# Kernel tuning notes

Hardware: AMD Instinct MI355X
Metric: run time of the kernel (lower is better)

The kernel has to match this reference:

```python
import jax, jax.numpy as jnp
import numpy as np

POOL = 14  # pool_size


def setup_inputs() -> dict:
    key = jax.random.key(0)
    k1, k2, k3, k4, k5 = jax.random.split(key, 5)
    H = W = 128
    C = 1024
    R = 256  # num_rois
    img = jax.random.normal(k1, (1, H, W, C), dtype=jnp.float32)
    # valid integer boxes (x1,y1,x2,y2) with x2>x1, y2>y1, inside the map
    x1 = jax.random.randint(k2, (R,), 0, W // 2)
    y1 = jax.random.randint(k3, (R,), 0, H // 2)
    bw = jax.random.randint(k4, (R,), 4, W // 2)
    bh = jax.random.randint(k5, (R,), 4, H // 2)
    rois = jnp.stack([x1, y1, x1 + bw, y1 + bh], axis=1).astype(jnp.float32)[None]  # [1,R,4]
    return {"img": img, "rois": rois}


def _roi_resize(img, rois, pool):
    # img: [1,H,W,C], rois: [1,R,4] float (x1,y1,x2,y2)
    H, W = img.shape[1], img.shape[2]
    fmap = img[0]  # [H,W,C]
    r = rois[0].astype(jnp.int32)  # cast exactly as the Keras layer does
    x1, y1, x2, y2 = r[:, 0], r[:, 1], r[:, 2], r[:, 3]
    h = (y2 - y1).astype(jnp.float32)  # [R]
    w = (x2 - x1).astype(jnp.float32)
    i = jnp.arange(pool, dtype=jnp.float32)
    # TF1 resize_images bilinear, align_corners=False: src = dst * (in/out)
    src_y = i[None, :] * (h[:, None] / pool)  # [R,P]
    src_x = i[None, :] * (w[:, None] / pool)
    y0 = jnp.floor(src_y).astype(jnp.int32)
    x0 = jnp.floor(src_x).astype(jnp.int32)
    fy = src_y - y0.astype(jnp.float32)  # [R,P]
    fx = src_x - x0.astype(jnp.float32)
    y1i = jnp.minimum(y0 + 1, (y2 - y1)[:, None] - 1)  # clamp within crop
    x1i = jnp.minimum(x0 + 1, (x2 - x1)[:, None] - 1)
    # absolute indices into the feature map, clipped for safety
    ay0 = jnp.clip(y1[:, None] + y0, 0, H - 1)
    ay1 = jnp.clip(y1[:, None] + y1i, 0, H - 1)
    ax0 = jnp.clip(x1[:, None] + x0, 0, W - 1)
    ax1 = jnp.clip(x1[:, None] + x1i, 0, W - 1)
    # batched gather of the four bilinear corners: [R,P,P,C]
    v00 = fmap[ay0[:, :, None], ax0[:, None, :]]
    v01 = fmap[ay0[:, :, None], ax1[:, None, :]]
    v10 = fmap[ay1[:, :, None], ax0[:, None, :]]
    v11 = fmap[ay1[:, :, None], ax1[:, None, :]]
    fx_b = fx[:, None, :, None]  # [R,1,P,1]
    fy_b = fy[:, :, None, None]  # [R,P,1,1]
    top = v00 + (v01 - v00) * fx_b
    bot = v10 + (v11 - v10) * fx_b
    out = top + (bot - top) * fy_b  # [R,P,P,C]
    return out[None]  # [1,R,P,P,C]


def reference(img, rois):
    return _roi_resize(img, rois, POOL)
```

## Files before the change

kernel.cpp:

```cpp
#include <hip/hip_runtime.h>

#define POOL 14
#define IMG_H 128
#define IMG_W 128
#define IMG_C 1024
#define NROI 256

typedef __attribute__((ext_vector_type(4))) float float4v;

__global__ __launch_bounds__(256) void roi_resize_kernel(
    const float* __restrict__ img,
    const float* __restrict__ rois,
    float* __restrict__ out)
{
    const int d    = blockIdx.x;
    const int xcd  = d & 7;
    const int slot = d >> 3;
    const int rwi  = slot / (POOL * POOL);
    const int pix  = slot - rwi * (POOL * POOL);
    const int r    = rwi * 8 + xcd;
    const int i    = pix / POOL;
    const int j    = pix - i * POOL;

    const int x1 = (int)rois[r * 4 + 0];
    const int y1 = (int)rois[r * 4 + 1];
    const int x2 = (int)rois[r * 4 + 2];
    const int y2 = (int)rois[r * 4 + 3];
    const int h = y2 - y1;
    const int w = x2 - x1;

    const float src_y = (float)i * ((float)h / (float)POOL);
    const float src_x = (float)j * ((float)w / (float)POOL);
    const int y0 = (int)floorf(src_y);
    const int x0 = (int)floorf(src_x);
    const float fy = src_y - (float)y0;
    const float fx = src_x - (float)x0;
    const int y1i = min(y0 + 1, h - 1);
    const int x1i = min(x0 + 1, w - 1);
    const int ay0 = min(max(y1 + y0,  0), IMG_H - 1);
    const int ay1 = min(max(y1 + y1i, 0), IMG_H - 1);
    const int ax0 = min(max(x1 + x0,  0), IMG_W - 1);
    const int ax1 = min(max(x1 + x1i, 0), IMG_W - 1);

    const float* p00 = img + (size_t)(ay0 * IMG_W + ax0) * IMG_C;
    const float* p01 = img + (size_t)(ay0 * IMG_W + ax1) * IMG_C;
    const float* p10 = img + (size_t)(ay1 * IMG_W + ax0) * IMG_C;
    const float* p11 = img + (size_t)(ay1 * IMG_W + ax1) * IMG_C;
    float* po = out + ((size_t)r * (POOL * POOL) + pix) * IMG_C;

    const int c = threadIdx.x * 4;

    const float4v v00 = *(const float4v*)(p00 + c);
    const float4v v01 = *(const float4v*)(p01 + c);
    const float4v v10 = *(const float4v*)(p10 + c);
    const float4v v11 = *(const float4v*)(p11 + c);

    float4v o;
    #pragma unroll
    for (int k = 0; k < 4; ++k) {
        const float top = v00[k] + (v01[k] - v00[k]) * fx;
        const float bot = v10[k] + (v11[k] - v10[k]) * fx;
        o[k] = top + (bot - top) * fy;
    }
    *(float4v*)(po + c) = o;
}

extern "C" void kernel_launch(void* const* d_in, const int* in_sizes, int n_in,
                              void* d_out, int out_size, void* d_ws, size_t ws_size,
                              hipStream_t stream) {
    const float* img  = (const float*)d_in[0];
    const float* rois = (const float*)d_in[1];
    float* out = (float*)d_out;

    const int pixels = NROI * POOL * POOL;
    roi_resize_kernel<<<pixels, 256, 0, stream>>>(img, rois, out);
}
```

Measured before the change: 302.6 us.

## Process one output row per block and use nontemporal stores

Each block now handles a full output row of 14 pixels for one ROI instead of a single pixel, looping over columns. This cuts the block count by 14x and amortizes the ROI and row index setup across the row. Output writes become nontemporal stores so the large streaming output does not pollute the cache. Fewer blocks lowers parallelism per pixel and serializes loads within each thread, which could limit memory-level parallelism.

```diff
diff --git a/kernel.cpp b/kernel.cpp
--- a/kernel.cpp
+++ b/kernel.cpp
@@ -16,11 +16,9 @@
     const int d    = blockIdx.x;
     const int xcd  = d & 7;
     const int slot = d >> 3;
-    const int rwi  = slot / (POOL * POOL);
-    const int pix  = slot - rwi * (POOL * POOL);
+    const int rwi  = slot / POOL;
+    const int i    = slot - rwi * POOL;
     const int r    = rwi * 8 + xcd;
-    const int i    = pix / POOL;
-    const int j    = pix - i * POOL;
 
     const int x1 = (int)rois[r * 4 + 0];
     const int y1 = (int)rois[r * 4 + 1];
@@ -30,39 +28,43 @@
     const int w = x2 - x1;
 
     const float src_y = (float)i * ((float)h / (float)POOL);
-    const float src_x = (float)j * ((float)w / (float)POOL);
     const int y0 = (int)floorf(src_y);
-    const int x0 = (int)floorf(src_x);
     const float fy = src_y - (float)y0;
-    const float fx = src_x - (float)x0;
     const int y1i = min(y0 + 1, h - 1);
-    const int x1i = min(x0 + 1, w - 1);
     const int ay0 = min(max(y1 + y0,  0), IMG_H - 1);
     const int ay1 = min(max(y1 + y1i, 0), IMG_H - 1);
-    const int ax0 = min(max(x1 + x0,  0), IMG_W - 1);
-    const int ax1 = min(max(x1 + x1i, 0), IMG_W - 1);
 
-    const float* p00 = img + (size_t)(ay0 * IMG_W + ax0) * IMG_C;
-    const float* p01 = img + (size_t)(ay0 * IMG_W + ax1) * IMG_C;
-    const float* p10 = img + (size_t)(ay1 * IMG_W + ax0) * IMG_C;
-    const float* p11 = img + (size_t)(ay1 * IMG_W + ax1) * IMG_C;
-    float* po = out + ((size_t)r * (POOL * POOL) + pix) * IMG_C;
+    const float* row0 = img + (size_t)(ay0 * IMG_W) * IMG_C;
+    const float* row1 = img + (size_t)(ay1 * IMG_W) * IMG_C;
 
     const int c = threadIdx.x * 4;
+    float* po = out + ((size_t)r * (POOL * POOL) + (size_t)i * POOL) * IMG_C + c;
 
-    const float4v v00 = *(const float4v*)(p00 + c);
-    const float4v v01 = *(const float4v*)(p01 + c);
-    const float4v v10 = *(const float4v*)(p10 + c);
-    const float4v v11 = *(const float4v*)(p11 + c);
+    const float winv = (float)w / (float)POOL;
 
-    float4v o;
-    #pragma unroll
-    for (int k = 0; k < 4; ++k) {
-        const float top = v00[k] + (v01[k] - v00[k]) * fx;
-        const float bot = v10[k] + (v11[k] - v10[k]) * fx;
-        o[k] = top + (bot - top) * fy;
+    #pragma unroll 2
+    for (int j = 0; j < POOL; ++j) {
+        const float src_x = (float)j * winv;
+        const int x0 = (int)floorf(src_x);
+        const float fx = src_x - (float)x0;
+        const int x1i = min(x0 + 1, w - 1);
+        const int ax0 = min(max(x1 + x0,  0), IMG_W - 1);
+        const int ax1 = min(max(x1 + x1i, 0), IMG_W - 1);
+
+        const float4v v00 = *(const float4v*)(row0 + (size_t)ax0 * IMG_C + c);
+        const float4v v01 = *(const float4v*)(row0 + (size_t)ax1 * IMG_C + c);
+        const float4v v10 = *(const float4v*)(row1 + (size_t)ax0 * IMG_C + c);
+        const float4v v11 = *(const float4v*)(row1 + (size_t)ax1 * IMG_C + c);
+
+        float4v o;
+        #pragma unroll
+        for (int k = 0; k < 4; ++k) {
+            const float top = v00[k] + (v01[k] - v00[k]) * fx;
+            const float bot = v10[k] + (v11[k] - v10[k]) * fx;
+            o[k] = top + (bot - top) * fy;
+        }
+        __builtin_nontemporal_store(o, (float4v*)(po + (size_t)j * IMG_C));
     }
-    *(float4v*)(po + c) = o;
 }
 
 extern "C" void kernel_launch(void* const* d_in, const int* in_sizes, int n_in,
@@ -72,6 +74,6 @@
     const float* rois = (const float*)d_in[1];
     float* out = (float*)d_out;
 
-    const int pixels = NROI * POOL * POOL;
-    roi_resize_kernel<<<pixels, 256, 0, stream>>>(img, rois, out);
+    const int blocks = NROI * POOL;
+    roi_resize_kernel<<<blocks, 256, 0, stream>>>(img, rois, out);
 }
```

Result: no change. 298.5 us (-1.3%).
